# Performance work log

Measured on AMD Instinct MI355X. Metric: run time of the kernel, lower is better.

Reference implementation:

```python
import jax, jax.numpy as jnp
import numpy as np

TAU = 1.0
EPS = 1e-8  # torch cosine_similarity norm clamp


def setup_inputs() -> dict:
    key = jax.random.key(0)
    k1, k2, k3 = jax.random.split(key, 3)
    B, d, M, C = 4096, 128, 8192, 16
    f = jax.random.normal(k1, (B, d), dtype=jnp.float32)
    f_neg = jax.random.normal(k2, (M, d), dtype=jnp.float32)
    labels = jax.random.randint(k3, (B,), 0, C, dtype=jnp.int64)
    return {"f": f, "f_neg": f_neg, "labels": labels, "batch_size": B}


def _normalize(x):
    n = jnp.linalg.norm(x, axis=-1, keepdims=True)
    return x / jnp.maximum(n, EPS)


def reference(f, f_neg, labels, batch_size):
    B = batch_size
    fn = _normalize(f)            # [B, d]
    gn = _normalize(f_neg)        # [M, d]

    sim_bb = jnp.einsum('id,jd->ij', fn, fn)   # [B, B] cosine sims in-batch
    sim_bn = jnp.einsum('id,md->im', fn, gn)   # [B, M] sims with neg bank

    offdiag = ~jnp.eye(B, dtype=bool)                       # exclude self
    pos_mask = (labels[:, None] == labels[None, :]) & offdiag  # [B, B]

    exp_bb = jnp.exp(sim_bb / TAU) * offdiag                # self row removed
    exp_bn = jnp.exp(sim_bn / TAU)
    # denominator_i = sum over all non-self in-batch + all bank negatives
    denom = exp_bb.sum(axis=1) + exp_bn.sum(axis=1)         # [B]

    # -log(exp(s_p/tau)/denom) = log(denom) - s_p/tau, averaged over positives
    neg_log = jnp.log(denom)[:, None] - sim_bb / TAU        # [B, B]
    n_pos = pos_mask.sum(axis=1)                            # [B]
    loss_i = jnp.sum(jnp.where(pos_mask, neg_log, 0.0), axis=1) / n_pos

    return jnp.sum(loss_i) / B  # reduction='mean'
```

## Files before the change

### kernel.cpp

```cpp
#include <hip/hip_runtime.h>
#include <hip/hip_bf16.h>
#include <hip/hip_fp8.h>

#define B_ROWS 4096
#define D_K    128
#define M_ROWS 8192
#define N_TOT  12288
#define NCHUNK 32
#define JT_PER_CHUNK 6
#define JCOLS  64
#define NCLS   16

typedef __attribute__((ext_vector_type(4))) int   intx4;
typedef __attribute__((ext_vector_type(8))) int   intx8;
typedef __attribute__((ext_vector_type(4))) float floatx4;

__device__ __forceinline__ float fp8_to_f32(unsigned char b) {
    __hip_fp8_e4m3 h; h.__x = b; return float(h);
}

__global__ __launch_bounds__(256) void nrm_kernel(
    const float* __restrict__ f, const float* __restrict__ fneg,
    unsigned char* __restrict__ G8, unsigned char* __restrict__ A8,
    float* __restrict__ S, int* __restrict__ hist, float* __restrict__ out)
{
    const int tid  = threadIdx.x;
    const int wave = tid >> 6;
    const int lane = tid & 63;
    const int row  = blockIdx.x * 4 + wave;
    if (blockIdx.x == 0) {
        #pragma unroll
        for (int k = 0; k < 8; ++k) S[tid + k * 256] = 0.f;
        if (tid < NCLS) hist[tid] = 0;
        if (tid == 0) out[0] = 0.f;
    }
    const float* src = (row < B_ROWS) ? (f + (size_t)row * D_K)
                                      : (fneg + (size_t)(row - B_ROWS) * D_K);
    float2 v = *reinterpret_cast<const float2*>(src + lane * 2);
    float ss = v.x * v.x + v.y * v.y;
    #pragma unroll
    for (int m = 1; m < 64; m <<= 1) ss += __shfl_xor(ss, m, 64);
    const float scale = 1.0f / fmaxf(sqrtf(ss), 1e-8f);
    __hip_fp8_e4m3 q0(v.x * scale);
    __hip_fp8_e4m3 q1(v.y * scale);
    const unsigned short pk =
        (unsigned short)q0.__x | ((unsigned short)q1.__x << 8);
    *reinterpret_cast<unsigned short*>(G8 + (size_t)row * D_K + lane * 2) = pk;
    if (row < B_ROWS) {
        const float s2 = scale * 1.44269504f;
        __hip_fp8_e4m3 a0(v.x * s2);
        __hip_fp8_e4m3 a1(v.y * s2);
        const unsigned short pa =
            (unsigned short)a0.__x | ((unsigned short)a1.__x << 8);
        *reinterpret_cast<unsigned short*>(A8 + (size_t)row * D_K + lane * 2) = pa;
    }
}

__global__ __launch_bounds__(256, 2) void sim_kernel(
    const unsigned char* __restrict__ G8, const unsigned char* __restrict__ A8,
    const int* __restrict__ labels, float* __restrict__ part_d,
    float* __restrict__ S, int* __restrict__ hist)
{
    __shared__ unsigned char Bs[2][JCOLS * D_K];

    const int tid = threadIdx.x;

    if (blockIdx.y >= 32) {
        const int svc    = (blockIdx.y - 32) * NCHUNK + blockIdx.x;
        const int stripe = svc & 31;
        const int dc     = svc >> 5;
        float* Sp = (float*)&Bs[0][0];
        int*   lh = (int*)(Sp + NCLS * 32);
        for (int k = tid; k < NCLS * 32; k += 256) Sp[k] = 0.f;
        if (tid < NCLS) lh[tid] = 0;
        __syncthreads();

        const int j0 = stripe * 128;
        if (dc == 0 && tid < 128) atomicAdd(&lh[labels[j0 + tid]], 1);

        const int d = tid & 31;
        const int w = tid >> 5;
        for (int jj = w; jj < 128; jj += 8) {
            const int j = j0 + jj;
            const int c = labels[j];
            atomicAdd(&Sp[c * 32 + d],
                      fp8_to_f32(G8[(size_t)j * D_K + dc * 32 + d]));
        }
        __syncthreads();
        for (int k = tid; k < NCLS * 32; k += 256)
            atomicAdd(&S[(k >> 5) * D_K + dc * 32 + (k & 31)], Sp[k]);
        if (dc == 0 && tid < NCLS) atomicAdd(&hist[tid], lh[tid]);
        return;
    }

    const int jc   = blockIdx.x;
    const int it   = blockIdx.y;
    const int wave = tid >> 6;
    const int lane = tid & 63;
    const int i0   = it * 128 + wave * 32;

    const int r16 = lane & 15;
    const int grp = lane >> 4;

    const unsigned char* Abase = A8 + (size_t)(i0 + r16) * D_K + grp * 32;
    intx8 afr[2];
    #pragma unroll
    for (int a = 0; a < 2; ++a)
        afr[a] = *reinterpret_cast<const intx8*>(Abase + (size_t)a * 16 * D_K);

    float dsum[2][4];
    #pragma unroll
    for (int a = 0; a < 2; ++a)
        #pragma unroll
        for (int r = 0; r < 4; ++r) dsum[a][r] = 0.f;

    int srcoff[2];
    #pragma unroll
    for (int s = 0; s < 2; ++s) {
        const int row  = s * 32 + (tid >> 3);
        const int gran = (tid & 7) ^ ((row >> 2) & 1);
        srcoff[s] = row * D_K + gran * 16;
    }

    intx4 streg[2];
    {
        const unsigned char* src =
            G8 + (size_t)(jc * JT_PER_CHUNK) * JCOLS * D_K;
        #pragma unroll
        for (int s = 0; s < 2; ++s)
            streg[s] = *reinterpret_cast<const intx4*>(src + srcoff[s]);
        #pragma unroll
        for (int s = 0; s < 2; ++s)
            *reinterpret_cast<intx4*>(&Bs[0][0] + s * 4096 + tid * 16) =
                streg[s];
    }

    for (int t = 0; t < JT_PER_CHUNK; ++t) {
        const int cur = t & 1;
        __syncthreads();

        if (t + 1 < JT_PER_CHUNK) {
            const unsigned char* src =
                G8 + (size_t)(jc * JT_PER_CHUNK + t + 1) * JCOLS * D_K;
            #pragma unroll
            for (int s = 0; s < 2; ++s)
                streg[s] = *reinterpret_cast<const intx4*>(src + srcoff[s]);
        }

        floatx4 acc[2][4];
        #pragma unroll
        for (int a = 0; a < 2; ++a)
            #pragma unroll
            for (int b = 0; b < 4; ++b)
                acc[a][b] = (floatx4){0.f, 0.f, 0.f, 0.f};

        const unsigned char* base = &Bs[cur][0];
        #pragma unroll
        for (int b = 0; b < 4; ++b) {
            const int jloc = b * 16 + r16;
            const int sw   = (jloc >> 2) & 1;
            intx4 lo = *reinterpret_cast<const intx4*>(
                base + jloc * D_K + ((2 * grp)     ^ sw) * 16);
            intx4 hi = *reinterpret_cast<const intx4*>(
                base + jloc * D_K + ((2 * grp + 1) ^ sw) * 16);
            intx8 bfr;
            if (sw) { intx4 tmp = lo; lo = hi; hi = tmp; }
            #pragma unroll
            for (int e = 0; e < 4; ++e) { bfr[e] = lo[e]; bfr[e + 4] = hi[e]; }
            #pragma unroll
            for (int a = 0; a < 2; ++a)
                acc[a][b] = __builtin_amdgcn_mfma_scale_f32_16x16x128_f8f6f4(
                    afr[a], bfr, acc[a][b], 0, 0,
                    0, 0x7F7F7F7F, 0, 0x7F7F7F7F);
        }

        #pragma unroll
        for (int a = 0; a < 2; ++a)
            #pragma unroll
            for (int r = 0; r < 4; ++r) {
                float s0 = exp2f(acc[a][0][r]) + exp2f(acc[a][1][r]);
                float s1 = exp2f(acc[a][2][r]) + exp2f(acc[a][3][r]);
                dsum[a][r] += s0 + s1;
            }

        if (t + 1 < JT_PER_CHUNK) {
            #pragma unroll
            for (int s = 0; s < 2; ++s)
                *reinterpret_cast<intx4*>(
                    &Bs[cur ^ 1][0] + s * 4096 + tid * 16) = streg[s];
        }
    }

    #pragma unroll
    for (int a = 0; a < 2; ++a)
        #pragma unroll
        for (int r = 0; r < 4; ++r) {
            #pragma unroll
            for (int m = 1; m < 16; m <<= 1)
                dsum[a][r] += __shfl_xor(dsum[a][r], m, 64);
        }
    if (r16 == 0) {
        #pragma unroll
        for (int a = 0; a < 2; ++a)
            #pragma unroll
            for (int r = 0; r < 4; ++r)
                part_d[(size_t)(i0 + a * 16 + grp * 4 + r) * NCHUNK + jc] =
                    dsum[a][r];
    }
}

__global__ __launch_bounds__(256) void fin_kernel(
    const unsigned char* __restrict__ G8, const float* __restrict__ part_d,
    const float* __restrict__ S, const int* __restrict__ labels,
    const int* __restrict__ hist, float* __restrict__ out)
{
    const int tid  = threadIdx.x;
    const int wave = tid >> 6;
    const int lane = tid & 63;

    float lsum = 0.f;
    #pragma unroll 2
    for (int rr = 0; rr < 8; ++rr) {
        const int i   = (blockIdx.x * 4 + wave) * 8 + rr;
        const int lab = labels[i];
        float pd = (lane < NCHUNK) ? part_d[(size_t)i * NCHUNK + lane] : 0.f;
        const unsigned char* gr = G8 + (size_t)i * D_K + lane * 2;
        const float f0 = fp8_to_f32(gr[0]);
        const float f1 = fp8_to_f32(gr[1]);
        float2 sv = *reinterpret_cast<const float2*>(S + lab * D_K + lane * 2);
        float self = f0 * f0 + f1 * f1;
        float sp   = f0 * sv.x + f1 * sv.y;
        #pragma unroll
        for (int m = 1; m < 64; m <<= 1) {
            pd   += __shfl_xor(pd, m, 64);
            self += __shfl_xor(self, m, 64);
            sp   += __shfl_xor(sp, m, 64);
        }
        if (lane == 0) {
            const float npos  = (float)(hist[lab] - 1);
            const float denom = pd - __expf(self);
            lsum += __logf(denom) - (sp - self) / npos;
        }
    }
    __shared__ float w4[4];
    if (lane == 0) w4[wave] = lsum;
    __syncthreads();
    if (tid == 0)
        atomicAdd(out, (w4[0] + w4[1] + w4[2] + w4[3]) * (1.0f / (float)B_ROWS));
}

extern "C" void kernel_launch(void* const* d_in, const int* in_sizes, int n_in,
                              void* d_out, int out_size, void* d_ws, size_t ws_size,
                              hipStream_t stream) {
    const float* f      = (const float*)d_in[0];
    const float* fneg   = (const float*)d_in[1];
    const int*   labels = (const int*)d_in[2];
    float*       out    = (float*)d_out;

    char* ws = (char*)d_ws;
    unsigned char* G8     = (unsigned char*)(ws);
    unsigned char* A8     = (unsigned char*)(ws + 1572864);
    float*         part_d = (float*)(ws + 1572864 + 524288);
    float*         S      = (float*)(ws + 1572864 + 524288 + 524288);
    int*           hist   = (int*)(ws + 1572864 + 524288 + 524288 + 8192);

    nrm_kernel<<<N_TOT / 4, 256, 0, stream>>>(f, fneg, G8, A8, S, hist, out);

    dim3 gridS(NCHUNK, 36);
    sim_kernel<<<gridS, 256, 0, stream>>>(G8, A8, labels, part_d, S, hist);

    fin_kernel<<<128, 256, 0, stream>>>(G8, part_d, S, labels, hist, out);
}
```

Before: 36.11 us.

## Stage B tiles via direct global-to-LDS loads with wider tiles and new swizzle

Replaces the register-staged global→LDS copy of the negative-bank tile with global_load_lds direct transfers, doubles the column tile to 128 and halves the tile count per chunk, and changes the LDS XOR swizzle to an 8-way pattern. The per-tile exp2 reduction is now interleaved right after each MFMA pair instead of batched at the end. The aim is to cut VGPR staging traffic and ds_write instructions and to reduce bank conflicts. The LDS buffer must be sized for 128 columns, and the async loads depend on correct wait/barrier ordering.

```diff
diff --git a/kernel.cpp b/kernel.cpp
--- a/kernel.cpp
+++ b/kernel.cpp
@@ -7,8 +7,8 @@
 #define M_ROWS 8192
 #define N_TOT  12288
 #define NCHUNK 32
-#define JT_PER_CHUNK 6
-#define JCOLS  64
+#define JT_PER_CHUNK 3
+#define JCOLS  128
 #define NCLS   16
 
 typedef __attribute__((ext_vector_type(4))) int   intx4;
@@ -17,6 +17,12 @@
 
 __device__ __forceinline__ float fp8_to_f32(unsigned char b) {
     __hip_fp8_e4m3 h; h.__x = b; return float(h);
+}
+
+__device__ __forceinline__ void load_lds16(const unsigned char* g, unsigned char* l) {
+    __builtin_amdgcn_global_load_lds(
+        (const __attribute__((address_space(1))) void*)g,
+        (__attribute__((address_space(3))) void*)l, 16, 0, 0);
 }
 
 __global__ __launch_bounds__(256) void nrm_kernel(
@@ -114,25 +120,22 @@
         #pragma unroll
         for (int r = 0; r < 4; ++r) dsum[a][r] = 0.f;
 
-    int srcoff[2];
-    #pragma unroll
-    for (int s = 0; s < 2; ++s) {
-        const int row  = s * 32 + (tid >> 3);
-        const int gran = (tid & 7) ^ ((row >> 2) & 1);
+    int srcoff[4];
+    int dstoff[4];
+    #pragma unroll
+    for (int s = 0; s < 4; ++s) {
+        const int chunk = s * 4 + wave;
+        const int row   = chunk * 8 + (lane >> 3);
+        const int gran  = (lane & 7) ^ ((row >> 1) & 7);
         srcoff[s] = row * D_K + gran * 16;
-    }
-
-    intx4 streg[2];
+        dstoff[s] = chunk * 1024;
+    }
+
     {
-        const unsigned char* src =
-            G8 + (size_t)(jc * JT_PER_CHUNK) * JCOLS * D_K;
-        #pragma unroll
-        for (int s = 0; s < 2; ++s)
-            streg[s] = *reinterpret_cast<const intx4*>(src + srcoff[s]);
-        #pragma unroll
-        for (int s = 0; s < 2; ++s)
-            *reinterpret_cast<intx4*>(&Bs[0][0] + s * 4096 + tid * 16) =
-                streg[s];
+        const unsigned char* src = G8 + (size_t)(jc * JT_PER_CHUNK) * JCOLS * D_K;
+        #pragma unroll
+        for (int s = 0; s < 4; ++s)
+            load_lds16(src + srcoff[s], &Bs[0][dstoff[s]]);
     }
 
     for (int t = 0; t < JT_PER_CHUNK; ++t) {
@@ -143,51 +146,33 @@
             const unsigned char* src =
                 G8 + (size_t)(jc * JT_PER_CHUNK + t + 1) * JCOLS * D_K;
             #pragma unroll
-            for (int s = 0; s < 2; ++s)
-                streg[s] = *reinterpret_cast<const intx4*>(src + srcoff[s]);
-        }
-
-        floatx4 acc[2][4];
-        #pragma unroll
-        for (int a = 0; a < 2; ++a)
-            #pragma unroll
-            for (int b = 0; b < 4; ++b)
-                acc[a][b] = (floatx4){0.f, 0.f, 0.f, 0.f};
+            for (int s = 0; s < 4; ++s)
+                load_lds16(src + srcoff[s], &Bs[cur ^ 1][dstoff[s]]);
+        }
 
         const unsigned char* base = &Bs[cur][0];
         #pragma unroll
-        for (int b = 0; b < 4; ++b) {
+        for (int b = 0; b < 8; ++b) {
             const int jloc = b * 16 + r16;
-            const int sw   = (jloc >> 2) & 1;
-            intx4 lo = *reinterpret_cast<const intx4*>(
-                base + jloc * D_K + ((2 * grp)     ^ sw) * 16);
-            intx4 hi = *reinterpret_cast<const intx4*>(
-                base + jloc * D_K + ((2 * grp + 1) ^ sw) * 16);
+            const int sw   = (jloc >> 1) & 7;
+            const int a0   = jloc * D_K + (((2 * grp) ^ sw) * 16);
+            intx4 lo = *reinterpret_cast<const intx4*>(base + a0);
+            intx4 hi = *reinterpret_cast<const intx4*>(base + (a0 ^ 16));
+            if (sw & 1) { intx4 tmp = lo; lo = hi; hi = tmp; }
             intx8 bfr;
-            if (sw) { intx4 tmp = lo; lo = hi; hi = tmp; }
             #pragma unroll
             for (int e = 0; e < 4; ++e) { bfr[e] = lo[e]; bfr[e + 4] = hi[e]; }
+            floatx4 acc[2];
             #pragma unroll
             for (int a = 0; a < 2; ++a)
-                acc[a][b] = __builtin_amdgcn_mfma_scale_f32_16x16x128_f8f6f4(
-                    afr[a], bfr, acc[a][b], 0, 0,
+                acc[a] = __builtin_amdgcn_mfma_scale_f32_16x16x128_f8f6f4(
+                    afr[a], bfr, (floatx4){0.f, 0.f, 0.f, 0.f}, 0, 0,
                     0, 0x7F7F7F7F, 0, 0x7F7F7F7F);
-        }
-
-        #pragma unroll
-        for (int a = 0; a < 2; ++a)
-            #pragma unroll
-            for (int r = 0; r < 4; ++r) {
-                float s0 = exp2f(acc[a][0][r]) + exp2f(acc[a][1][r]);
-                float s1 = exp2f(acc[a][2][r]) + exp2f(acc[a][3][r]);
-                dsum[a][r] += s0 + s1;
-            }
-
-        if (t + 1 < JT_PER_CHUNK) {
-            #pragma unroll
-            for (int s = 0; s < 2; ++s)
-                *reinterpret_cast<intx4*>(
-                    &Bs[cur ^ 1][0] + s * 4096 + tid * 16) = streg[s];
+            #pragma unroll
+            for (int a = 0; a < 2; ++a)
+                #pragma unroll
+                for (int r = 0; r < 4; ++r)
+                    dsum[a][r] += exp2f(acc[a][r]);
         }
     }
 
```

Result: slower. 38.17 us (+5.7%).

## Precompute self-dots in normalize pass and regroup positive-term sum per class

Applied to the files above, without the earlier changes.

The normalize kernel now computes each batch row's fp8-quantized self dot product and its exponential, storing both. The final kernel no longer reads G8 rows or the per-class sums for every row. Instead, the positive-pair term is computed per class as (|S_c|^2 - sum of self dots)/(n_c-1) in 16 extra blocks. The per-row blocks only sum partial denominators and take the log. This removes per-row fp8 loads and dot products from the tail kernel, at the cost of extra reductions in the normalize kernel and 16 blocks that each scan all labels.

```diff
diff --git a/kernel.cpp b/kernel.cpp
--- a/kernel.cpp
+++ b/kernel.cpp
@@ -22,6 +22,7 @@
 __global__ __launch_bounds__(256) void nrm_kernel(
     const float* __restrict__ f, const float* __restrict__ fneg,
     unsigned char* __restrict__ G8, unsigned char* __restrict__ A8,
+    float* __restrict__ selfdot, float* __restrict__ expself,
     float* __restrict__ S, int* __restrict__ hist, float* __restrict__ out)
 {
     const int tid  = threadIdx.x;
@@ -53,6 +54,15 @@
         const unsigned short pa =
             (unsigned short)a0.__x | ((unsigned short)a1.__x << 8);
         *reinterpret_cast<unsigned short*>(A8 + (size_t)row * D_K + lane * 2) = pa;
+        const float d0 = fp8_to_f32((unsigned char)(pk & 0xff));
+        const float d1 = fp8_to_f32((unsigned char)(pk >> 8));
+        float sd = d0 * d0 + d1 * d1;
+        #pragma unroll
+        for (int m = 1; m < 64; m <<= 1) sd += __shfl_xor(sd, m, 64);
+        if (lane == 0) {
+            selfdot[row] = sd;
+            expself[row] = __expf(sd);
+        }
     }
 }
 
@@ -210,40 +220,65 @@
 }
 
 __global__ __launch_bounds__(256) void fin_kernel(
-    const unsigned char* __restrict__ G8, const float* __restrict__ part_d,
-    const float* __restrict__ S, const int* __restrict__ labels,
-    const int* __restrict__ hist, float* __restrict__ out)
+    const float* __restrict__ part_d, const float* __restrict__ S,
+    const int* __restrict__ labels, const int* __restrict__ hist,
+    const float* __restrict__ selfdot, const float* __restrict__ expself,
+    float* __restrict__ out)
 {
     const int tid  = threadIdx.x;
     const int wave = tid >> 6;
     const int lane = tid & 63;
-
+    __shared__ float w4[4];
+
+    if (blockIdx.x >= 256) {
+        const int c = blockIdx.x - 256;
+        float2 sv = *reinterpret_cast<const float2*>(S + c * D_K + lane * 2);
+        float dsq = sv.x * sv.x + sv.y * sv.y;
+        float tc  = 0.f;
+        for (int i = tid; i < B_ROWS; i += 256)
+            tc += (labels[i] == c) ? selfdot[i] : 0.f;
+        #pragma unroll
+        for (int m = 1; m < 64; m <<= 1) {
+            dsq += __shfl_xor(dsq, m, 64);
+            tc  += __shfl_xor(tc, m, 64);
+        }
+        __shared__ float wt[4];
+        if (lane == 0) { w4[wave] = dsq; wt[wave] = tc; }
+        __syncthreads();
+        if (tid == 0) {
+            const float Tc  = wt[0] + wt[1] + wt[2] + wt[3];
+            const float Dsq = w4[0];
+            const int   h   = hist[c];
+            if (h > 1)
+                atomicAdd(out, -((Dsq - Tc) / (float)(h - 1))
+                                  * (1.0f / (float)B_ROWS));
+        }
+        return;
+    }
+
+    const int i0 = (blockIdx.x * 4 + wave) * 4;
+    float pd[4];
+    #pragma unroll
+    for (int r = 0; r < 4; ++r)
+        pd[r] = (lane < NCHUNK)
+            ? part_d[(size_t)(i0 + r) * NCHUNK + lane] : 0.f;
+    float es[4];
+    #pragma unroll
+    for (int r = 0; r < 4; ++r) es[r] = expself[i0 + r];
+
+    #pragma unroll
+    for (int r = 0; r < 4; ++r) {
+        #pragma unroll
+        for (int m = 1; m < 32; m <<= 1)
+            pd[r] += __shfl_xor(pd[r], m, 64);
+    }
     float lsum = 0.f;
-    #pragma unroll 2
-    for (int rr = 0; rr < 8; ++rr) {
-        const int i   = (blockIdx.x * 4 + wave) * 8 + rr;
-        const int lab = labels[i];
-        float pd = (lane < NCHUNK) ? part_d[(size_t)i * NCHUNK + lane] : 0.f;
-        const unsigned char* gr = G8 + (size_t)i * D_K + lane * 2;
-        const float f0 = fp8_to_f32(gr[0]);
-        const float f1 = fp8_to_f32(gr[1]);
-        float2 sv = *reinterpret_cast<const float2*>(S + lab * D_K + lane * 2);
-        float self = f0 * f0 + f1 * f1;
-        float sp   = f0 * sv.x + f1 * sv.y;
-        #pragma unroll
-        for (int m = 1; m < 64; m <<= 1) {
-            pd   += __shfl_xor(pd, m, 64);
-            self += __shfl_xor(self, m, 64);
-            sp   += __shfl_xor(sp, m, 64);
-        }
-        if (lane == 0) {
-            const float npos  = (float)(hist[lab] - 1);
-            const float denom = pd - __expf(self);
-            lsum += __logf(denom) - (sp - self) / npos;
-        }
-    }
-    __shared__ float w4[4];
-    if (lane == 0) w4[wave] = lsum;
+    if (lane == 0) {
+        #pragma unroll
+        for (int r = 0; r < 4; ++r)
+            lsum += __logf(pd[r] - es[r]);
+        w4[wave] = lsum;
+    }
     __syncthreads();
     if (tid == 0)
         atomicAdd(out, (w4[0] + w4[1] + w4[2] + w4[3]) * (1.0f / (float)B_ROWS));
@@ -258,16 +293,20 @@
     float*       out    = (float*)d_out;
 
     char* ws = (char*)d_ws;
-    unsigned char* G8     = (unsigned char*)(ws);
-    unsigned char* A8     = (unsigned char*)(ws + 1572864);
-    float*         part_d = (float*)(ws + 1572864 + 524288);
-    float*         S      = (float*)(ws + 1572864 + 524288 + 524288);
-    int*           hist   = (int*)(ws + 1572864 + 524288 + 524288 + 8192);
-
-    nrm_kernel<<<N_TOT / 4, 256, 0, stream>>>(f, fneg, G8, A8, S, hist, out);
+    unsigned char* G8      = (unsigned char*)(ws);
+    unsigned char* A8      = (unsigned char*)(ws + 1572864);
+    float*         part_d  = (float*)(ws + 2097152);
+    float*         S       = (float*)(ws + 2621440);
+    int*           hist    = (int*)(ws + 2629632);
+    float*         selfdot = (float*)(ws + 2629696);
+    float*         expself = (float*)(ws + 2646080);
+
+    nrm_kernel<<<N_TOT / 4, 256, 0, stream>>>(f, fneg, G8, A8, selfdot,
+                                              expself, S, hist, out);
 
     dim3 gridS(NCHUNK, 36);
     sim_kernel<<<gridS, 256, 0, stream>>>(G8, A8, labels, part_d, S, hist);
 
-    fin_kernel<<<128, 256, 0, stream>>>(G8, part_d, S, labels, hist, out);
-}
+    fin_kernel<<<272, 256, 0, stream>>>(part_d, S, labels, hist, selfdot,
+                                        expself, out);
+}
```

After: 38.19 us. 5.7% more time.
